# Optimization experiments

Hardware: AMD Instinct MI355X
Metric: run time of the kernel (lower is better)

Reference implementation:

```python
import jax, jax.numpy as jnp
import numpy as np

KS = 31  # kernel size
PAD = KS // 2

def _dw_conv_plus_sum(x, w, C):
    # depthwise conv (groups=C, same padding) + global spatial-sum bias
    x_sum = jnp.sum(x, axis=(-2, -1), keepdims=True)
    y = jax.lax.conv_general_dilated(
        x, w,
        window_strides=(1, 1),
        padding=((PAD, PAD), (PAD, PAD)),
        dimension_numbers=('NCHW', 'OIHW', 'NCHW'),
        feature_group_count=C)
    return y + x_sum

def setup_inputs() -> dict:
    key = jax.random.key(0)
    k1, k2 = jax.random.split(key)
    bs, C, H, W = 16, 192, 64, 64
    qkv = jax.random.normal(k1, (bs, 3 * C, H * W), dtype=jnp.float32)
    weights = jax.random.normal(k2, (C, 1, KS, KS), dtype=jnp.float32) * 0.01
    return {"qkv": qkv, "weights": weights, "H": H, "W": W}

def reference(qkv, weights, H, W):
    bs, ch3, _ = qkv.shape
    C = ch3 // 3
    dtype = qkv.dtype
    x = qkv.reshape(bs, ch3, H, W).astype(jnp.float32)
    q, k, v = jnp.split(x, 3, axis=1)  # each (bs, C, H, W)
    # softmax over flattened spatial dims
    k = jax.nn.softmax(k.reshape(bs, C, H * W), axis=-1).reshape(bs, C, H, W)
    kv = k * v
    w = jnp.expm1(weights.astype(jnp.float32))  # (C,1,KS,KS)
    k_c = _dw_conv_plus_sum(k, w, C)
    kv_c = _dw_conv_plus_sum(kv, w, C)
    out = jax.nn.sigmoid(q) * kv_c / (k_c + 1e-8)
    return out.reshape(bs, C, H * W).astype(dtype)
```

## Files before the change

kernel.cpp:

```cpp
#include <hip/hip_runtime.h>
#include <math.h>


#define C_     192
#define BS_    16
#define HW_    4096
#define KS_    31
#define NT_    128

#define IROWS_ 94
#define ISTR_  104
#define IMGSZ_ (IROWS_ * ISTR_)
#define NFRAG_ 160
#define BF_PER_C_ (KS_ * NFRAG_ * 8)
#define BF_BYTES_ ((size_t)C_ * BF_PER_C_ * 2)

typedef _Float16 f16;
typedef _Float16 f16x4 __attribute__((ext_vector_type(4)));
typedef _Float16 f16x8 __attribute__((ext_vector_type(8)));
typedef float    f32x16 __attribute__((ext_vector_type(16)));

__global__ __launch_bounds__(256)
void build_bfrags(const float* __restrict__ wts, f16* __restrict__ bf)
{
    const int fi = blockIdx.x * 256 + threadIdx.x;
    if (fi >= C_ * KS_ * NFRAG_) return;
    const int s81 = fi % 80;
    int rest = fi / 80;
    const int l5 = rest & 1; rest >>= 1;
    const int dy = rest % KS_;
    const int c  = rest / KS_;
    const float* wrow = wts + (size_t)c * (KS_ * KS_) + dy * KS_;
    const int s = s81 - 31;
    f16x8 o;
#pragma unroll
    for (int j = 0; j < 8; ++j) {
        const int tap = s + 4 * l5 + (j & 3) + 8 * (j >> 2) - 1;
        o[j] = (tap >= 0 && tap < KS_) ? (f16)expm1f(wrow[tap]) : (f16)0.f;
    }
    *reinterpret_cast<f16x8*>(bf + (size_t)fi * 8) = o;
}

__global__ __launch_bounds__(NT_, 2)
void aft_mfma2(const float* __restrict__ qkv,
               const f16* __restrict__ bf,
               float* __restrict__ out)
{
    __shared__ __align__(16) f16 IMG[2 * IMGSZ_];
    __shared__ float red[8];

    const int blk = blockIdx.x;
    const int c = blk >> 4;
    const int b = blk & 15;
    const float* qrow = qkv + ((size_t)b * (3 * C_) + c) * HW_;
    const float* krow = qrow + (size_t)C_ * HW_;
    const float* vrow = qrow + (size_t)(2 * C_) * HW_;
    float*       orow = out + ((size_t)b * C_ + c) * HW_;

    const int t = threadIdx.x, lane = t & 63, wid = t >> 6;
    const int l5 = lane >> 5, l31 = lane & 31;

    uint4* I4 = reinterpret_cast<uint4*>(IMG);
    for (int i = t; i < (2 * IMGSZ_) / 8; i += NT_) I4[i] = make_uint4(0u, 0u, 0u, 0u);

    float pm = -3.0e38f;
#pragma unroll
    for (int i = 0; i < 8; ++i) {
        float4 k4 = ((const float4*)krow)[t + NT_ * i];
        pm = fmaxf(pm, fmaxf(fmaxf(k4.x, k4.y), fmaxf(k4.z, k4.w)));
    }
#pragma unroll
    for (int s = 32; s; s >>= 1) pm = fmaxf(pm, __shfl_xor(pm, s));
    if (lane == 0) red[wid] = pm;
    __syncthreads();
    const float m = fmaxf(red[0], red[1]);

    const int ry  = t >> 4;
    const int rx4 = t & 15;
    const int g   = 1 + (rx4 >> 2);
    const int q   = rx4 & 3;
    const int qp  = (q == 1) ? 2 : (q == 2) ? 1 : q;
    float zs = 0.f, skv = 0.f;
#pragma unroll
    for (int i = 0; i < 8; ++i) {
        float4 k4 = ((const float4*)krow)[t + NT_ * i];
        float4 v4 = ((const float4*)vrow)[t + NT_ * i];
        float e0 = __expf(k4.x - m), e1 = __expf(k4.y - m);
        float e2 = __expf(k4.z - m), e3 = __expf(k4.w - m);
        zs += (e0 + e1) + (e2 + e3);
        float a0 = e0 * v4.x, a1 = e1 * v4.y, a2 = e2 * v4.z, a3 = e3 * v4.w;
        skv += (a0 + a1) + (a2 + a3);
        const int row = ry + 8 * i + 15;
        f16* pE = (f16*)((char*)IMG + row * (ISTR_ * 2) + g * 32 + qp * 8);
        f16x4 he; he[0] = (f16)e0; he[1] = (f16)e1; he[2] = (f16)e2; he[3] = (f16)e3;
        f16x4 hk; hk[0] = (f16)a0; hk[1] = (f16)a1; hk[2] = (f16)a2; hk[3] = (f16)a3;
        *reinterpret_cast<f16x4*>(pE) = he;
        *reinterpret_cast<f16x4*>(pE + IMGSZ_) = hk;
    }
#pragma unroll
    for (int s = 32; s; s >>= 1) { zs += __shfl_xor(zs, s); skv += __shfl_xor(skv, s); }
    if (lane == 0) { red[2 + wid] = zs; red[4 + wid] = skv; }
    __syncthreads();
    const float Z     = red[2] + red[3];
    const float sumkv = red[4] + red[5];

    f32x16 aE0, aE1, aK0, aK1;
#pragma unroll
    for (int r = 0; r < 16; ++r) { aE0[r] = 0.f; aE1[r] = 0.f; aK0[r] = 0.f; aK1[r] = 0.f; }

    const f16* bl = bf + (size_t)c * BF_PER_C_ + l5 * 640 + (31 - l31) * 8;
    int abyte = ((32 * wid) + l31) * (ISTR_ * 2) + l5 * 16;

    f16x8 Bc[4];
#pragma unroll
    for (int kc = 0; kc < 4; ++kc)
        Bc[kc] = *reinterpret_cast<const f16x8*>(bl + kc * 128);

#pragma unroll 1
    for (int dy = 0; dy < KS_; ++dy) {
        const int dyn = (dy + 1 < KS_) ? dy + 1 : dy;
        const f16* bln = bl + dyn * (NFRAG_ * 8);
        f16x8 Bn[4];
#pragma unroll
        for (int kc = 0; kc < 4; ++kc)
            Bn[kc] = *reinterpret_cast<const f16x8*>(bln + kc * 128);

        f16x8 AE[6], AK[6];
        const char* ap = (const char*)IMG + abyte;
#pragma unroll
        for (int cc = 0; cc < 6; ++cc) {
            AE[cc] = *reinterpret_cast<const f16x8*>(ap + cc * 32);
            AK[cc] = *reinterpret_cast<const f16x8*>(ap + cc * 32 + IMGSZ_ * 2);
        }
#pragma unroll
        for (int kc = 0; kc < 4; ++kc) {
            aE0 = __builtin_amdgcn_mfma_f32_32x32x16_f16(AE[kc],     Bc[kc], aE0, 0, 0, 0);
            aE1 = __builtin_amdgcn_mfma_f32_32x32x16_f16(AE[kc + 2], Bc[kc], aE1, 0, 0, 0);
            aK0 = __builtin_amdgcn_mfma_f32_32x32x16_f16(AK[kc],     Bc[kc], aK0, 0, 0, 0);
            aK1 = __builtin_amdgcn_mfma_f32_32x32x16_f16(AK[kc + 2], Bc[kc], aK1, 0, 0, 0);
        }
#pragma unroll
        for (int kc = 0; kc < 4; ++kc) Bc[kc] = Bn[kc];
        abyte += ISTR_ * 2;
    }

    const int yb = 32 * wid + 4 * l5;
#pragma unroll
    for (int tt = 0; tt < 2; ++tt) {
        const f32x16& ke = tt ? aE1 : aE0;
        const f32x16& kv = tt ? aK1 : aK0;
        const int x = 32 * tt + l31;
#pragma unroll
        for (int r = 0; r < 16; ++r) {
            const int y = yb + (r & 3) + 8 * (r >> 2);
            const int idx = y * 64 + x;
            const float qv = qrow[idx];
            const float den = (ke[r] + Z + Z * 1e-8f) * (1.f + __expf(-qv));
            orow[idx] = (kv[r] + sumkv) * __builtin_amdgcn_rcpf(den);
        }
    }
}

#define FB_IROWS_ 94
#define FB_ISTR_  100
#define FB_WCOLS_ 96

__device__ __forceinline__ void conv_pass_fb(const f16* __restrict__ img,
                                             const unsigned int* __restrict__ wp,
                                             int lane, int ybase,
                                             f32x16* acc0, f32x16* acc1)
{
    const int l5  = lane >> 5;
    const int l31 = lane & 31;
    int aoff = (ybase + l31) * FB_ISTR_ + 4 * l5;
    const unsigned int* bp0 = wp + (32 + 4 * l5 - l31);
#pragma unroll 1
    for (int dy = 0; dy < KS_; ++dy) {
        f16x8 A[6];
        const f16* ap = img + aoff;
#pragma unroll
        for (int cc = 0; cc < 6; ++cc) {
            f16x4 lo = *(const f16x4*)(ap + cc * 16);
            f16x4 hi = *(const f16x4*)(ap + cc * 16 + 8);
            A[cc] = __builtin_shufflevector(lo, hi, 0, 1, 2, 3, 4, 5, 6, 7);
        }
        const unsigned int* bp = bp0 + dy * FB_WCOLS_;
#pragma unroll
        for (int kc = 0; kc < 4; ++kc) {
            uint4 bw;
            bw.x = bp[kc * 16 + 0];
            bw.y = bp[kc * 16 + 2];
            bw.z = bp[kc * 16 + 8];
            bw.w = bp[kc * 16 + 10];
            f16x8 B = __builtin_bit_cast(f16x8, bw);
            *acc0 = __builtin_amdgcn_mfma_f32_32x32x16_f16(A[kc],     B, *acc0, 0, 0, 0);
            *acc1 = __builtin_amdgcn_mfma_f32_32x32x16_f16(A[kc + 2], B, *acc1, 0, 0, 0);
        }
        aoff += FB_ISTR_;
    }
}

__global__ __launch_bounds__(NT_, 2)
void aft_mfma(const float* __restrict__ qkv,
              const float* __restrict__ wts,
              float* __restrict__ out)
{
    __shared__ __align__(16) f16 IMGF[FB_IROWS_ * FB_ISTR_];
    __shared__ unsigned int WP[KS_ * FB_WCOLS_];
    __shared__ float red[8];

    const int bc = blockIdx.x;
    const int b  = bc / C_;
    const int c  = bc - b * C_;
    const float* qrow = qkv + ((size_t)b * (3 * C_) + c) * HW_;
    const float* krow = qrow + (size_t)C_ * HW_;
    const float* vrow = qrow + (size_t)(2 * C_) * HW_;
    float*       orow = out + ((size_t)b * C_ + c) * HW_;

    const int t = threadIdx.x, lane = t & 63, wid = t >> 6;

    unsigned int* IMGu = (unsigned int*)IMGF;
    for (int i = t; i < (FB_IROWS_ * FB_ISTR_) / 2; i += NT_) IMGu[i] = 0u;
    const float* wch = wts + (size_t)c * (KS_ * KS_);
    for (int i = t; i < KS_ * FB_WCOLS_; i += NT_) {
        const int dy = i / FB_WCOLS_, cw = i - dy * FB_WCOLS_;
        const int d0 = cw - 33, d1 = cw - 32;
        const float w0 = (d0 >= 0 && d0 < KS_) ? expm1f(wch[dy * KS_ + d0]) : 0.f;
        const float w1 = (d1 >= 0 && d1 < KS_) ? expm1f(wch[dy * KS_ + d1]) : 0.f;
        union { unsigned int u; f16 h[2]; } pk;
        pk.h[0] = (f16)w0; pk.h[1] = (f16)w1;
        WP[i] = pk.u;
    }

    float kvv[32];
    float pm = -3.0e38f;
#pragma unroll
    for (int i = 0; i < 8; ++i) {
        float4 v = ((const float4*)krow)[t + NT_ * i];
        kvv[4*i+0] = v.x; kvv[4*i+1] = v.y; kvv[4*i+2] = v.z; kvv[4*i+3] = v.w;
        pm = fmaxf(pm, fmaxf(fmaxf(v.x, v.y), fmaxf(v.z, v.w)));
    }
#pragma unroll
    for (int s = 32; s; s >>= 1) pm = fmaxf(pm, __shfl_xor(pm, s));
    if (lane == 0) red[wid] = pm;
    __syncthreads();
    const float m = fmaxf(red[0], red[1]);

    const int ry = t >> 4;
    const int rx = (t & 15) * 4;
    float ps = 0.f;
#pragma unroll
    for (int i = 0; i < 8; ++i) {
        f16x4 h;
#pragma unroll
        for (int e = 0; e < 4; ++e) {
            float ev = __expf(kvv[4*i+e] - m);
            ps += ev;
            h[e] = (f16)ev;
        }
        *(f16x4*)(&IMGF[(ry + 8 * i + 15) * FB_ISTR_ + rx + 16]) = h;
    }
#pragma unroll
    for (int s = 32; s; s >>= 1) ps += __shfl_xor(ps, s);
    if (lane == 0) red[2 + wid] = ps;
    __syncthreads();
    const float Z = red[2] + red[3];

    f32x16 accA0, accA1;
#pragma unroll
    for (int r = 0; r < 16; ++r) { accA0[r] = 0.f; accA1[r] = 0.f; }
    conv_pass_fb(IMGF, WP, lane, 32 * wid, &accA0, &accA1);
    __syncthreads();

    float skv = 0.f;
#pragma unroll
    for (int i = 0; i < 8; ++i) {
        float4 v = ((const float4*)vrow)[t + NT_ * i];
        f16* pp = &IMGF[(ry + 8 * i + 15) * FB_ISTR_ + rx + 16];
        f16x4 h = *(f16x4*)pp;
        float a0 = (float)h[0] * v.x;
        float a1 = (float)h[1] * v.y;
        float a2 = (float)h[2] * v.z;
        float a3 = (float)h[3] * v.w;
        skv += (a0 + a1) + (a2 + a3);
        h[0] = (f16)a0; h[1] = (f16)a1; h[2] = (f16)a2; h[3] = (f16)a3;
        *(f16x4*)pp = h;
    }
#pragma unroll
    for (int s = 32; s; s >>= 1) skv += __shfl_xor(skv, s);
    if (lane == 0) red[4 + wid] = skv;
    __syncthreads();
    const float sumkv = red[4] + red[5];

    f32x16 accB0, accB1;
#pragma unroll
    for (int r = 0; r < 16; ++r) { accB0[r] = 0.f; accB1[r] = 0.f; }
    conv_pass_fb(IMGF, WP, lane, 32 * wid, &accB0, &accB1);

    const int yb = 32 * wid + 4 * (lane >> 5);
    const int l31 = lane & 31;
#pragma unroll
    for (int tt = 0; tt < 2; ++tt) {
        const f32x16& ka = tt ? accA1 : accA0;
        const f32x16& va = tt ? accB1 : accB0;
        const int x = 32 * tt + l31;
#pragma unroll
        for (int r = 0; r < 16; ++r) {
            const int y = yb + (r & 3) + 8 * (r >> 2);
            const int idx = y * 64 + x;
            const float qv = qrow[idx];
            const float den = (ka[r] + Z + Z * 1e-8f) * (1.f + __expf(-qv));
            orow[idx] = (va[r] + sumkv) * __builtin_amdgcn_rcpf(den);
        }
    }
}

extern "C" void kernel_launch(void* const* d_in, const int* in_sizes, int n_in,
                              void* d_out, int out_size, void* d_ws, size_t ws_size,
                              hipStream_t stream)
{
    const float* qkv = (const float*)d_in[0];
    const float* wts = (const float*)d_in[1];
    float* out       = (float*)d_out;
    (void)in_sizes; (void)n_in; (void)out_size;

    if (ws_size >= BF_BYTES_ && d_ws != nullptr) {
        f16* bfr = (f16*)d_ws;
        const int total = C_ * KS_ * NFRAG_;
        build_bfrags<<<dim3((total + 255) / 256), dim3(256), 0, stream>>>(wts, bfr);
        aft_mfma2<<<dim3(BS_ * C_), dim3(NT_), 0, stream>>>(qkv, bfr, out);
    } else {
        aft_mfma<<<dim3(BS_ * C_), dim3(NT_), 0, stream>>>(qkv, wts, out);
    }
}
```

Baseline: 308.3 us.

## Split conv dy range across 4 waves with LDS reduction and XCD-aware block remap

Doubles the block to 256 threads. Each pair of waves now covers half of the 31 kernel-row taps, and the partial MFMA accumulators are then combined through LDS before the epilogue. Block IDs are also remapped so consecutive work items spread across XCDs. The aim is more parallelism per image and more latency hiding on the MFMA loop. The cost is an extra LDS reduction and barriers, an uneven 16/15 dy split, and possible register or occupancy pressure from the 4-wave launch bound.

Result: faster. 282.9 us (-8.2%).

```diff
diff --git a/kernel.cpp b/kernel.cpp
--- a/kernel.cpp
+++ b/kernel.cpp
@@ -6,7 +6,7 @@
 #define BS_    16
 #define HW_    4096
 #define KS_    31
-#define NT_    128
+#define NT_    256
 
 #define IROWS_ 94
 #define ISTR_  104
@@ -41,17 +41,18 @@
     *reinterpret_cast<f16x8*>(bf + (size_t)fi * 8) = o;
 }
 
-__global__ __launch_bounds__(NT_, 2)
-void aft_mfma2(const float* __restrict__ qkv,
+__global__ __launch_bounds__(NT_, 4)
+void aft_mfma3(const float* __restrict__ qkv,
                const f16* __restrict__ bf,
                float* __restrict__ out)
 {
     __shared__ __align__(16) f16 IMG[2 * IMGSZ_];
-    __shared__ float red[8];
-
-    const int blk = blockIdx.x;
-    const int c = blk >> 4;
-    const int b = blk & 15;
+    __shared__ float red[12];
+
+    const int bid  = blockIdx.x;
+    const int work = (bid & 7) * (BS_ * C_ / 8) + (bid >> 3);
+    const int c = work >> 4;
+    const int b = work & 15;
     const float* qrow = qkv + ((size_t)b * (3 * C_) + c) * HW_;
     const float* krow = qrow + (size_t)C_ * HW_;
     const float* vrow = qrow + (size_t)(2 * C_) * HW_;
@@ -65,7 +66,7 @@
 
     float pm = -3.0e38f;
 #pragma unroll
-    for (int i = 0; i < 8; ++i) {
+    for (int i = 0; i < 4; ++i) {
         float4 k4 = ((const float4*)krow)[t + NT_ * i];
         pm = fmaxf(pm, fmaxf(fmaxf(k4.x, k4.y), fmaxf(k4.z, k4.w)));
     }
@@ -73,7 +74,7 @@
     for (int s = 32; s; s >>= 1) pm = fmaxf(pm, __shfl_xor(pm, s));
     if (lane == 0) red[wid] = pm;
     __syncthreads();
-    const float m = fmaxf(red[0], red[1]);
+    const float m = fmaxf(fmaxf(red[0], red[1]), fmaxf(red[2], red[3]));
 
     const int ry  = t >> 4;
     const int rx4 = t & 15;
@@ -82,7 +83,7 @@
     const int qp  = (q == 1) ? 2 : (q == 2) ? 1 : q;
     float zs = 0.f, skv = 0.f;
 #pragma unroll
-    for (int i = 0; i < 8; ++i) {
+    for (int i = 0; i < 4; ++i) {
         float4 k4 = ((const float4*)krow)[t + NT_ * i];
         float4 v4 = ((const float4*)vrow)[t + NT_ * i];
         float e0 = __expf(k4.x - m), e1 = __expf(k4.y - m);
@@ -90,7 +91,7 @@
         zs += (e0 + e1) + (e2 + e3);
         float a0 = e0 * v4.x, a1 = e1 * v4.y, a2 = e2 * v4.z, a3 = e3 * v4.w;
         skv += (a0 + a1) + (a2 + a3);
-        const int row = ry + 8 * i + 15;
+        const int row = ry + 16 * i + 15;
         f16* pE = (f16*)((char*)IMG + row * (ISTR_ * 2) + g * 32 + qp * 8);
         f16x4 he; he[0] = (f16)e0; he[1] = (f16)e1; he[2] = (f16)e2; he[3] = (f16)e3;
         f16x4 hk; hk[0] = (f16)a0; hk[1] = (f16)a1; hk[2] = (f16)a2; hk[3] = (f16)a3;
@@ -99,26 +100,31 @@
     }
 #pragma unroll
     for (int s = 32; s; s >>= 1) { zs += __shfl_xor(zs, s); skv += __shfl_xor(skv, s); }
-    if (lane == 0) { red[2 + wid] = zs; red[4 + wid] = skv; }
-    __syncthreads();
-    const float Z     = red[2] + red[3];
-    const float sumkv = red[4] + red[5];
+    if (lane == 0) { red[4 + wid] = zs; red[8 + wid] = skv; }
+    __syncthreads();
+    const float Z     = (red[4] + red[5]) + (red[6] + red[7]);
+    const float sumkv = (red[8] + red[9]) + (red[10] + red[11]);
+
+    const int rowhalf = wid & 1;
+    const int dyh     = wid >> 1;
+    const int dy0     = dyh * 16;
+    const int dyEnd   = dyh ? KS_ : 16;
 
     f32x16 aE0, aE1, aK0, aK1;
 #pragma unroll
     for (int r = 0; r < 16; ++r) { aE0[r] = 0.f; aE1[r] = 0.f; aK0[r] = 0.f; aK1[r] = 0.f; }
 
     const f16* bl = bf + (size_t)c * BF_PER_C_ + l5 * 640 + (31 - l31) * 8;
-    int abyte = ((32 * wid) + l31) * (ISTR_ * 2) + l5 * 16;
+    int abyte = (32 * rowhalf + l31 + dy0) * (ISTR_ * 2) + l5 * 16;
 
     f16x8 Bc[4];
 #pragma unroll
     for (int kc = 0; kc < 4; ++kc)
-        Bc[kc] = *reinterpret_cast<const f16x8*>(bl + kc * 128);
+        Bc[kc] = *reinterpret_cast<const f16x8*>(bl + dy0 * (NFRAG_ * 8) + kc * 128);
 
 #pragma unroll 1
-    for (int dy = 0; dy < KS_; ++dy) {
-        const int dyn = (dy + 1 < KS_) ? dy + 1 : dy;
+    for (int dy = dy0; dy < dyEnd; ++dy) {
+        const int dyn = (dy + 1 < dyEnd) ? dy + 1 : dy;
         const f16* bln = bl + dyn * (NFRAG_ * 8);
         f16x8 Bn[4];
 #pragma unroll
@@ -143,20 +149,48 @@
         for (int kc = 0; kc < 4; ++kc) Bc[kc] = Bn[kc];
         abyte += ISTR_ * 2;
     }
-
-    const int yb = 32 * wid + 4 * l5;
-#pragma unroll
-    for (int tt = 0; tt < 2; ++tt) {
-        const f32x16& ke = tt ? aE1 : aE0;
-        const f32x16& kv = tt ? aK1 : aK0;
-        const int x = 32 * tt + l31;
+    __syncthreads();
+
+    float* REDU = (float*)IMG;
+    if (wid >= 2) {
+        float* p = REDU + ((wid - 2) * 64 + lane) * 68;
+        const float* a0 = (const float*)&aE0;
+        const float* a1 = (const float*)&aE1;
+        const float* a2 = (const float*)&aK0;
+        const float* a3 = (const float*)&aK1;
+#pragma unroll
+        for (int j2 = 0; j2 < 4; ++j2) {
+            ((float4*)p)[j2 + 0]  = ((const float4*)a0)[j2];
+            ((float4*)p)[j2 + 4]  = ((const float4*)a1)[j2];
+            ((float4*)p)[j2 + 8]  = ((const float4*)a2)[j2];
+            ((float4*)p)[j2 + 12] = ((const float4*)a3)[j2];
+        }
+    }
+    __syncthreads();
+    if (wid < 2) {
+        const float* p = REDU + (wid * 64 + lane) * 68;
 #pragma unroll
         for (int r = 0; r < 16; ++r) {
-            const int y = yb + (r & 3) + 8 * (r >> 2);
-            const int idx = y * 64 + x;
-            const float qv = qrow[idx];
-            const float den = (ke[r] + Z + Z * 1e-8f) * (1.f + __expf(-qv));
-            orow[idx] = (kv[r] + sumkv) * __builtin_amdgcn_rcpf(den);
+            aE0[r] += p[r];
+            aE1[r] += p[16 + r];
+            aK0[r] += p[32 + r];
+            aK1[r] += p[48 + r];
+        }
+
+        const int yb = 32 * rowhalf + 4 * l5;
+#pragma unroll
+        for (int tt = 0; tt < 2; ++tt) {
+            const f32x16& ke = tt ? aE1 : aE0;
+            const f32x16& kv = tt ? aK1 : aK0;
+            const int x = 32 * tt + l31;
+#pragma unroll
+            for (int r = 0; r < 16; ++r) {
+                const int y = yb + (r & 3) + 8 * (r >> 2);
+                const int idx = y * 64 + x;
+                const float qv = qrow[idx];
+                const float den = (ke[r] + Z + Z * 1e-8f) * (1.f + __expf(-qv));
+                orow[idx] = (kv[r] + sumkv) * __builtin_amdgcn_rcpf(den);
+            }
         }
     }
 }
@@ -200,7 +234,7 @@
     }
 }
 
-__global__ __launch_bounds__(NT_, 2)
+__global__ __launch_bounds__(128, 2)
 void aft_mfma(const float* __restrict__ qkv,
               const float* __restrict__ wts,
               float* __restrict__ out)
@@ -220,9 +254,9 @@
     const int t = threadIdx.x, lane = t & 63, wid = t >> 6;
 
     unsigned int* IMGu = (unsigned int*)IMGF;
-    for (int i = t; i < (FB_IROWS_ * FB_ISTR_) / 2; i += NT_) IMGu[i] = 0u;
+    for (int i = t; i < (FB_IROWS_ * FB_ISTR_) / 2; i += 128) IMGu[i] = 0u;
     const float* wch = wts + (size_t)c * (KS_ * KS_);
-    for (int i = t; i < KS_ * FB_WCOLS_; i += NT_) {
+    for (int i = t; i < KS_ * FB_WCOLS_; i += 128) {
         const int dy = i / FB_WCOLS_, cw = i - dy * FB_WCOLS_;
         const int d0 = cw - 33, d1 = cw - 32;
         const float w0 = (d0 >= 0 && d0 < KS_) ? expm1f(wch[dy * KS_ + d0]) : 0.f;
@@ -236,7 +270,7 @@
     float pm = -3.0e38f;
 #pragma unroll
     for (int i = 0; i < 8; ++i) {
-        float4 v = ((const float4*)krow)[t + NT_ * i];
+        float4 v = ((const float4*)krow)[t + 128 * i];
         kvv[4*i+0] = v.x; kvv[4*i+1] = v.y; kvv[4*i+2] = v.z; kvv[4*i+3] = v.w;
         pm = fmaxf(pm, fmaxf(fmaxf(v.x, v.y), fmaxf(v.z, v.w)));
     }
@@ -275,7 +309,7 @@
     float skv = 0.f;
 #pragma unroll
     for (int i = 0; i < 8; ++i) {
-        float4 v = ((const float4*)vrow)[t + NT_ * i];
+        float4 v = ((const float4*)vrow)[t + 128 * i];
         f16* pp = &IMGF[(ry + 8 * i + 15) * FB_ISTR_ + rx + 16];
         f16x4 h = *(f16x4*)pp;
         float a0 = (float)h[0] * v.x;
@@ -328,8 +362,8 @@
         f16* bfr = (f16*)d_ws;
         const int total = C_ * KS_ * NFRAG_;
         build_bfrags<<<dim3((total + 255) / 256), dim3(256), 0, stream>>>(wts, bfr);
-        aft_mfma2<<<dim3(BS_ * C_), dim3(NT_), 0, stream>>>(qkv, bfr, out);
+        aft_mfma3<<<dim3(BS_ * C_), dim3(NT_), 0, stream>>>(qkv, bfr, out);
     } else {
-        aft_mfma<<<dim3(BS_ * C_), dim3(NT_), 0, stream>>>(qkv, wts, out);
-    }
-}
+        aft_mfma<<<dim3(BS_ * C_), dim3(128), 0, stream>>>(qkv, wts, out);
+    }
+}
```
